# Kernel optimization log

Measured on AMD Instinct MI355X. Metric: run time of the kernel, lower is better.

The kernel has to match this reference:

```python
import math
import jax, jax.numpy as jnp
import numpy as np

DILATIONS = (1, 2, 3)

def conv2d(x, w, b, d=1, p=0):
    # x: NCHW, w: OIHW
    y = jax.lax.conv_general_dilated(
        x, w, window_strides=(1, 1), padding=[(p, p), (p, p)],
        rhs_dilation=(d, d), dimension_numbers=('NCHW', 'OIHW', 'NCHW'))
    return y + b[None, :, None, None]

def setup_inputs() -> dict:
    key = jax.random.key(0)
    ks = jax.random.split(key, 6)
    B, C, H = 2, 256, 96
    inner = 256 // 18  # = 14
    f = lambda k, s, sc: jax.random.normal(k, s, dtype=jnp.float32) * sc
    return {
        'x':        f(ks[0], (B, C, H, H), 1.0),
        'proj_w':   f(ks[1], (C, C, 1, 1), 0.06),
        'proj_b':   jnp.zeros((C,), jnp.float32),
        'reduce_w': f(ks[2], (inner, C, 1, 1), 0.06),
        'reduce_b': jnp.zeros((inner,), jnp.float32),
        'dil_w':    f(ks[3], (3, inner, inner, 3, 3), 0.08),
        'dil_b':    jnp.zeros((3, inner), jnp.float32),
        'fuse_w':   f(ks[4], (C, inner * 3 * 6, 1, 1), 0.06),
        'fuse_b':   jnp.zeros((C,), jnp.float32),
    }

def reference(x, proj_w, proj_b, reduce_w, reduce_b, dil_w, dil_b, fuse_w, fuse_b):
    B, C, H, W = x.shape
    # PatchEmbed (1x1 conv, stride 1) then PatchUnEmbed is identity on layout
    fmap = conv2d(x, proj_w, proj_b)                    # (B,C,H,W)
    # SAMSNLMFilter
    xr = conv2d(fmap, reduce_w, reduce_b)               # (B,inner,H,W)
    tfs = [xr,
           jnp.flip(xr, -1),
           jnp.flip(xr, -2),
           jnp.rot90(xr, 1, (-2, -1)),
           jnp.rot90(xr, 2, (-2, -1)),
           jnp.rot90(xr, 3, (-2, -1))]
    feats = []
    for i, d in enumerate(DILATIONS):
        co = conv2d(xr, dil_w[i], dil_b[i], d=d, p=d)   # (B,inner,H,W)
        feats.extend(co * t for t in tfs)
    fused = conv2d(jnp.concatenate(feats, axis=1), fuse_w, fuse_b)  # (B,C,H,W)
    tok = fused.reshape(B, C, H * W).transpose(0, 2, 1)             # (B,N,C)
    scale = 1.0 / math.sqrt(C)
    scores = jnp.einsum('bnc,bmc->bnm', tok, tok) * scale           # (B,N,N)
    attn = jax.nn.softmax(scores, axis=-1)
    out = jnp.einsum('bnm,bmc->bnc', attn, tok)
    out = out.transpose(0, 2, 1).reshape(B, C, H, W)
    return fmap + 0.2 * out  # residual_scale default 0.2
```

## Files before the change

kernel.cpp:

```cpp
#include <hip/hip_runtime.h>
#include <hip/hip_bf16.h>

#define NB 2
#define CH 256
#define HS 96
#define HW 9216
#define CHW 2359296
#define INNER 14
#define NF 252
#define SCALE 0.0625f

using f32x4 = __attribute__((ext_vector_type(4))) float;
using s16x8 = __attribute__((ext_vector_type(8))) short;

template<int CIN, typename OT>
__global__ __launch_bounds__(256)
void k_conv1x1(const float* __restrict__ in, const float* __restrict__ w,
               const float* __restrict__ bias, OT* __restrict__ out) {
    __shared__ float wsh[CIN][32];
    const int tid = threadIdx.x;
    const int coB = blockIdx.y * 32;
    for (int e = tid; e < CIN * 32; e += 256) {
        int ci = e >> 5, col = e & 31;
        wsh[ci][col] = w[(coB + col) * CIN + ci];
    }
    __syncthreads();
    const int P0  = blockIdx.x * 512 + tid;
    const int b   = P0 / HW;
    const int pp0 = P0 - b * HW;
    const int pp1 = pp0 + 256;
    const float* inb = in + (size_t)b * CIN * HW;
    float acc0[32], acc1[32];
    #pragma unroll
    for (int j = 0; j < 32; ++j) { acc0[j] = 0.f; acc1[j] = 0.f; }
    for (int ci = 0; ci < CIN; ++ci) {
        float x0 = inb[(size_t)ci * HW + pp0];
        float x1 = inb[(size_t)ci * HW + pp1];
        const float4* wr = (const float4*)wsh[ci];
        #pragma unroll
        for (int q = 0; q < 8; ++q) {
            float4 wv = wr[q];
            acc0[q*4+0] += wv.x*x0; acc0[q*4+1] += wv.y*x0;
            acc0[q*4+2] += wv.z*x0; acc0[q*4+3] += wv.w*x0;
            acc1[q*4+0] += wv.x*x1; acc1[q*4+1] += wv.y*x1;
            acc1[q*4+2] += wv.z*x1; acc1[q*4+3] += wv.w*x1;
        }
    }
    OT* ob = out + (size_t)b * CH * HW;
    #pragma unroll
    for (int j = 0; j < 32; ++j) {
        float bv = bias[coB + j];
        ob[(size_t)(coB + j) * HW + pp0] = (OT)(acc0[j] + bv);
        ob[(size_t)(coB + j) * HW + pp1] = (OT)(acc1[j] + bv);
    }
}

__global__ __launch_bounds__(64)
void k_reduce(const float* __restrict__ fmap, const float* __restrict__ w,
              const float* __restrict__ bias, float* __restrict__ xr) {
    __shared__ float wsh[256][16];
    const int tid = threadIdx.x;
    for (int e = tid; e < 256 * 16; e += 64) {
        int ci = e >> 4, co = e & 15;
        wsh[ci][co] = (co < INNER) ? w[co * 256 + ci] : 0.f;
    }
    __syncthreads();
    const int P  = blockIdx.x * 64 + tid;
    const int b  = P / HW;
    const int pp = P - b * HW;
    const float* fb = fmap + (size_t)b * CHW;
    float acc[16];
    #pragma unroll
    for (int j = 0; j < 16; ++j) acc[j] = 0.f;
    for (int ci = 0; ci < 256; ++ci) {
        float xv = fb[(size_t)ci * HW + pp];
        const float4* wr = (const float4*)wsh[ci];
        #pragma unroll
        for (int q = 0; q < 4; ++q) {
            float4 wv = wr[q];
            acc[q*4+0] += wv.x*xv; acc[q*4+1] += wv.y*xv;
            acc[q*4+2] += wv.z*xv; acc[q*4+3] += wv.w*xv;
        }
    }
    float* xb = xr + (size_t)b * INNER * HW;
    #pragma unroll
    for (int co = 0; co < INNER; ++co)
        xb[(size_t)co * HW + pp] = acc[co] + bias[co];
}

__global__ __launch_bounds__(256)
void k_dil(const float* __restrict__ xr, const float* __restrict__ dw,
           const float* __restrict__ db, float* __restrict__ feats) {
    int bid = blockIdx.x;
    const int hb = bid % 36; bid /= 36;
    const int oc = bid % 14; bid /= 14;
    const int b  = bid & 1;  bid >>= 1;
    const int d  = bid;
    const int dil = d + 1;
    __shared__ float wsh[126];
    const int tid = threadIdx.x;
    if (tid < 126) wsh[tid] = dw[(d * 14 + oc) * 126 + tid];
    __syncthreads();
    const int p = hb * 256 + tid;
    const int h = p / 96, w = p - (p / 96) * 96;
    const float* xb = xr + (size_t)b * INNER * HW;
    float acc = db[d * 14 + oc];
    for (int ic = 0; ic < 14; ++ic) {
        const float* xc = xb + (size_t)ic * HW;
        #pragma unroll
        for (int kh = 0; kh < 3; ++kh) {
            int ih = h + (kh - 1) * dil;
            if (ih < 0 || ih >= 96) continue;
            #pragma unroll
            for (int kw = 0; kw < 3; ++kw) {
                int iw = w + (kw - 1) * dil;
                if (iw < 0 || iw >= 96) continue;
                acc += xc[ih * 96 + iw] * wsh[ic * 9 + kh * 3 + kw];
            }
        }
    }
    const float* xo = xb + (size_t)oc * HW;
    const int H1 = 95;
    float t0 = xo[h * 96 + w];
    float t1 = xo[h * 96 + (H1 - w)];
    float t2 = xo[(H1 - h) * 96 + w];
    float t3 = xo[w * 96 + (H1 - h)];
    float t4 = xo[(H1 - h) * 96 + (H1 - w)];
    float t5 = xo[(H1 - w) * 96 + h];
    float* fo = feats + (size_t)b * NF * HW;
    const int ch0 = d * 6 * 14 + oc;
    fo[(size_t)(ch0 + 0 * 14) * HW + p] = acc * t0;
    fo[(size_t)(ch0 + 1 * 14) * HW + p] = acc * t1;
    fo[(size_t)(ch0 + 2 * 14) * HW + p] = acc * t2;
    fo[(size_t)(ch0 + 3 * 14) * HW + p] = acc * t3;
    fo[(size_t)(ch0 + 4 * 14) * HW + p] = acc * t4;
    fo[(size_t)(ch0 + 5 * 14) * HW + p] = acc * t5;
}

__global__ __launch_bounds__(256)
void k_tr(const unsigned short* __restrict__ tc, unsigned short* __restrict__ tt) {
    const int tid = threadIdx.x;
    int bid = blockIdx.x;
    const int b = bid / 576;
    const int r = bid - b * 576;
    const int t0 = (r >> 2) * 64;
    const int c0 = (r & 3) * 64;
    __shared__ unsigned int T[64][37];
    const unsigned short* tcb = tc + (size_t)b * CHW;
    unsigned short* ttb = tt + (size_t)b * CHW;
    for (int e = tid; e < 2048; e += 256) {
        int to = e & 63, chp = e >> 6;
        unsigned int v0 = tcb[(size_t)(c0 + 2*chp)     * HW + t0 + to];
        unsigned int v1 = tcb[(size_t)(c0 + 2*chp + 1) * HW + t0 + to];
        T[to][chp] = (v1 << 16) | v0;
    }
    __syncthreads();
    for (int e = tid; e < 2048; e += 256) {
        int to = e >> 5, chp = e & 31;
        ((unsigned int*)(ttb + (size_t)(t0 + to) * CH + c0))[chp] = T[to][chp];
    }
}

#define KTILE 64
#define NKT 144

__device__ __forceinline__ unsigned int pk_bf16(float lo, float hi) {
    unsigned int l = __bfloat16_as_ushort(__float2bfloat16(lo));
    unsigned int h = __bfloat16_as_ushort(__float2bfloat16(hi));
    return (h << 16) | l;
}

__global__ __launch_bounds__(256, 2)
void k_attn2(const unsigned short* __restrict__ tok_t,
             const unsigned short* __restrict__ tok_c,
             const float* __restrict__ fmap, float* __restrict__ outp) {
    __shared__ unsigned short Kt[64][256];
    __shared__ unsigned short Vt[256][64];
    __shared__ unsigned short Psh[4][16][72];
    const int tid  = threadIdx.x;
    const int wid  = tid >> 6;
    const int lane = tid & 63;
    const int lq   = lane & 15;
    const int lg   = lane >> 4;

    const int blk = blockIdx.x;
    const int qb  = (blk & 7) * 36 + (blk >> 3);
    const int b   = qb / 144;
    const int q0  = (qb - b * 144) * 64;
    const unsigned short* tt = tok_t + (size_t)b * CHW;
    const unsigned short* tc = tok_c + (size_t)b * CHW;

    s16x8 qf[8];
    {
        const unsigned short* qrow = tt + (size_t)(q0 + wid*16 + lq) * CH + 8*lg;
        #pragma unroll
        for (int ks = 0; ks < 8; ++ks)
            qf[ks] = *(const s16x8*)(qrow + 32*ks);
    }
    float m_r = -1e30f, l_r = 0.f;
    f32x4 oacc[16];
    #pragma unroll
    for (int ct = 0; ct < 16; ++ct) oacc[ct] = (f32x4){0.f,0.f,0.f,0.f};

    for (int t = 0; t < NKT; ++t) {
        const int k0 = t * KTILE;
        __syncthreads();
        for (int c = tid; c < 2048; c += 256) {
            int key = c >> 5, cho = (c & 31) * 8;
            s16x8 v = *(const s16x8*)(tt + (size_t)(k0 + key) * CH + cho);
            *(s16x8*)(&Kt[key][cho ^ ((key & 7) << 3)]) = v;
        }
        for (int c = tid; c < 2048; c += 256) {
            int ch = c >> 3, ko = (c & 7) * 8;
            s16x8 v = *(const s16x8*)(tc + (size_t)ch * HW + k0 + ko);
            *(s16x8*)(&Vt[ch][ko ^ ((ch & 7) << 3)]) = v;
        }
        __syncthreads();

        float s[16];
        #pragma unroll
        for (int mt = 0; mt < 4; ++mt) {
            f32x4 acc = (f32x4){0.f,0.f,0.f,0.f};
            const int key = mt * 16 + lq;
            const int sw  = (key & 7) << 3;
            #pragma unroll
            for (int ks = 0; ks < 8; ++ks) {
                s16x8 af = *(const s16x8*)(&Kt[key][(ks*32 + 8*lg) ^ sw]);
                acc = __builtin_amdgcn_mfma_f32_16x16x32_bf16(af, qf[ks], acc, 0, 0, 0);
            }
            #pragma unroll
            for (int r = 0; r < 4; ++r) s[mt*4 + r] = acc[r] * SCALE;
        }
        float tm = s[0];
        #pragma unroll
        for (int i = 1; i < 16; ++i) tm = fmaxf(tm, s[i]);
        tm = fmaxf(tm, __shfl_xor(tm, 16));
        tm = fmaxf(tm, __shfl_xor(tm, 32));
        const float mn = fmaxf(m_r, tm);
        const float alpha = __expf(m_r - mn);
        m_r = mn;
        float ps = 0.f;
        #pragma unroll
        for (int i = 0; i < 16; ++i) { s[i] = __expf(s[i] - mn); ps += s[i]; }
        ps += __shfl_xor(ps, 16);
        ps += __shfl_xor(ps, 32);
        l_r = l_r * alpha + ps;
        #pragma unroll
        for (int ct = 0; ct < 16; ++ct) {
            oacc[ct][0] *= alpha; oacc[ct][1] *= alpha;
            oacc[ct][2] *= alpha; oacc[ct][3] *= alpha;
        }
        #pragma unroll
        for (int kt = 0; kt < 4; ++kt) {
            *(unsigned int*)&Psh[wid][lq][16*kt + 4*lg]     = pk_bf16(s[kt*4+0], s[kt*4+1]);
            *(unsigned int*)&Psh[wid][lq][16*kt + 4*lg + 2] = pk_bf16(s[kt*4+2], s[kt*4+3]);
        }
        s16x8 pb0 = *(const s16x8*)&Psh[wid][lq][8*lg];
        s16x8 pb1 = *(const s16x8*)&Psh[wid][lq][32 + 8*lg];
        #pragma unroll
        for (int ct = 0; ct < 16; ++ct) {
            const int ch = ct * 16 + lq;
            const int sw = (ch & 7) << 3;
            s16x8 va0 = *(const s16x8*)(&Vt[ch][(8*lg) ^ sw]);
            s16x8 va1 = *(const s16x8*)(&Vt[ch][(32 + 8*lg) ^ sw]);
            oacc[ct] = __builtin_amdgcn_mfma_f32_16x16x32_bf16(va0, pb0, oacc[ct], 0, 0, 0);
            oacc[ct] = __builtin_amdgcn_mfma_f32_16x16x32_bf16(va1, pb1, oacc[ct], 0, 0, 0);
        }
    }
    const float linv = 1.f / l_r;
    const float* fb = fmap + (size_t)b * CHW;
    float* ob = outp + (size_t)b * CHW;
    const int qg = q0 + wid * 16 + lq;
    #pragma unroll
    for (int ct = 0; ct < 16; ++ct)
        #pragma unroll
        for (int cr = 0; cr < 4; ++cr) {
            const int ch = ct * 16 + 4 * lg + cr;
            const size_t g = (size_t)ch * HW + qg;
            ob[g] = fb[g] + 0.2f * (oacc[ct][cr] * linv);
        }
}

extern "C" void kernel_launch(void* const* d_in, const int* in_sizes, int n_in,
                              void* d_out, int out_size, void* d_ws, size_t ws_size,
                              hipStream_t stream) {
    const float* x        = (const float*)d_in[0];
    const float* proj_w   = (const float*)d_in[1];
    const float* proj_b   = (const float*)d_in[2];
    const float* reduce_w = (const float*)d_in[3];
    const float* reduce_b = (const float*)d_in[4];
    const float* dil_w    = (const float*)d_in[5];
    const float* dil_b    = (const float*)d_in[6];
    const float* fuse_w   = (const float*)d_in[7];
    const float* fuse_b   = (const float*)d_in[8];
    float* out = (float*)d_out;

    float* ws    = (float*)d_ws;
    float* fmap  = ws;
    float* xr    = fmap + 4718592;
    float* feats = xr + 258048;
    unsigned short* tok_c = (unsigned short*)(feats + 4644864);
    unsigned short* tok_t = tok_c + 4718592;

    k_conv1x1<256, float><<<dim3(36, 8), 256, 0, stream>>>(x, proj_w, proj_b, fmap);
    k_reduce<<<288, 64, 0, stream>>>(fmap, reduce_w, reduce_b, xr);
    k_dil<<<3024, 256, 0, stream>>>(xr, dil_w, dil_b, feats);
    k_conv1x1<252, __hip_bfloat16><<<dim3(36, 8), 256, 0, stream>>>(
        feats, fuse_w, fuse_b, (__hip_bfloat16*)tok_c);
    k_tr<<<1152, 256, 0, stream>>>(tok_c, tok_t);
    k_attn2<<<288, 256, 0, stream>>>(tok_t, tok_c, fmap, out);
}
```

Baseline: 871.7 us.

## Double-buffer attention K/V tiles with direct global-to-LDS loads and lazy rescale

The attention kernel now double-buffers K and V tiles in LDS, filling them with global_load_lds asynchronous copies so the next tile's fetch overlaps the current tile's MFMA work, and it drops one barrier per iteration. Softmax switches to exp2 with a pre-folded log2e scale and only rescales the accumulators when the running max grows by more than a threshold. The reduce kernel is widened to 256 threads, splitting the channel loop four ways with an LDS reduction. Doubling LDS forces one block per CU (launch bounds lowered), which reduces occupancy, and the lazy-rescale threshold relies on fp32 headroom.

New measurement: 964.8 us. +10.7%, slower.

```diff
diff --git a/kernel.cpp b/kernel.cpp
--- a/kernel.cpp
+++ b/kernel.cpp
@@ -8,10 +8,17 @@
 #define CHW 2359296
 #define INNER 14
 #define NF 252
-#define SCALE 0.0625f
+#define SL2E 0.09016844f
 
 using f32x4 = __attribute__((ext_vector_type(4))) float;
 using s16x8 = __attribute__((ext_vector_type(8))) short;
+
+__device__ __forceinline__ void gload_lds16(const unsigned short* g, unsigned short* l) {
+    __builtin_amdgcn_global_load_lds(
+        (const __attribute__((address_space(1))) unsigned int*)g,
+        (__attribute__((address_space(3))) unsigned int*)l,
+        16, 0, 0);
+}
 
 template<int CIN, typename OT>
 __global__ __launch_bounds__(256)
@@ -55,26 +62,28 @@
     }
 }
 
-__global__ __launch_bounds__(64)
+__global__ __launch_bounds__(256)
 void k_reduce(const float* __restrict__ fmap, const float* __restrict__ w,
               const float* __restrict__ bias, float* __restrict__ xr) {
     __shared__ float wsh[256][16];
+    __shared__ float part[4][64][17];
     const int tid = threadIdx.x;
-    for (int e = tid; e < 256 * 16; e += 64) {
+    for (int e = tid; e < 256 * 16; e += 256) {
         int ci = e >> 4, co = e & 15;
         wsh[ci][co] = (co < INNER) ? w[co * 256 + ci] : 0.f;
     }
     __syncthreads();
-    const int P  = blockIdx.x * 64 + tid;
-    const int b  = P / HW;
-    const int pp = P - b * HW;
-    const float* fb = fmap + (size_t)b * CHW;
+    const int px  = tid & 63, grp = tid >> 6;
+    const int Pb  = blockIdx.x * 64;
+    const int b   = Pb / HW;
+    const int ppb = Pb - b * HW;
+    const float* fb = fmap + (size_t)b * CHW + (size_t)(grp * 64) * HW + ppb + px;
     float acc[16];
     #pragma unroll
     for (int j = 0; j < 16; ++j) acc[j] = 0.f;
-    for (int ci = 0; ci < 256; ++ci) {
-        float xv = fb[(size_t)ci * HW + pp];
-        const float4* wr = (const float4*)wsh[ci];
+    for (int ci = 0; ci < 64; ++ci) {
+        float xv = fb[(size_t)ci * HW];
+        const float4* wr = (const float4*)wsh[grp * 64 + ci];
         #pragma unroll
         for (int q = 0; q < 4; ++q) {
             float4 wv = wr[q];
@@ -82,10 +91,15 @@
             acc[q*4+2] += wv.z*xv; acc[q*4+3] += wv.w*xv;
         }
     }
-    float* xb = xr + (size_t)b * INNER * HW;
-    #pragma unroll
-    for (int co = 0; co < INNER; ++co)
-        xb[(size_t)co * HW + pp] = acc[co] + bias[co];
+    #pragma unroll
+    for (int j = 0; j < 16; ++j) part[grp][px][j] = acc[j];
+    __syncthreads();
+    for (int e = tid; e < 64 * INNER; e += 256) {
+        int co = e >> 6, p2 = e & 63;
+        float v = part[0][p2][co] + part[1][p2][co] + part[2][p2][co] +
+                  part[3][p2][co] + bias[co];
+        xr[(size_t)(b * INNER + co) * HW + ppb + p2] = v;
+    }
 }
 
 __global__ __launch_bounds__(256)
@@ -170,12 +184,12 @@
     return (h << 16) | l;
 }
 
-__global__ __launch_bounds__(256, 2)
+__global__ __launch_bounds__(256, 1)
 void k_attn2(const unsigned short* __restrict__ tok_t,
              const unsigned short* __restrict__ tok_c,
              const float* __restrict__ fmap, float* __restrict__ outp) {
-    __shared__ unsigned short Kt[64][256];
-    __shared__ unsigned short Vt[256][64];
+    __shared__ unsigned short Kt[2][64][256];
+    __shared__ unsigned short Vt[2][256][64];
     __shared__ unsigned short Psh[4][16][72];
     const int tid  = threadIdx.x;
     const int wid  = tid >> 6;
@@ -190,6 +204,18 @@
     const unsigned short* tt = tok_t + (size_t)b * CHW;
     const unsigned short* tc = tok_c + (size_t)b * CHW;
 
+    int koff[8], voff[8];
+    #pragma unroll
+    for (int i = 0; i < 8; ++i) {
+        int c   = i * 256 + tid;
+        int key = c >> 5, sc = c & 31;
+        koff[i] = key * CH + ((sc ^ (key & 7)) << 3);
+        int ch  = c >> 3, sv = c & 7;
+        voff[i] = ch * HW + ((sv ^ (ch & 7)) << 3);
+    }
+    unsigned short* KtF = &Kt[0][0][0];
+    unsigned short* VtF = &Vt[0][0][0];
+
     s16x8 qf[8];
     {
         const unsigned short* qrow = tt + (size_t)(q0 + wid*16 + lq) * CH + 8*lg;
@@ -202,21 +228,29 @@
     #pragma unroll
     for (int ct = 0; ct < 16; ++ct) oacc[ct] = (f32x4){0.f,0.f,0.f,0.f};
 
+    #pragma unroll
+    for (int i = 0; i < 8; ++i) {
+        int c = i * 256 + tid;
+        gload_lds16(tt + koff[i], KtF + c * 8);
+        gload_lds16(tc + voff[i], VtF + c * 8);
+    }
+    __syncthreads();
+
+    int cur = 0;
     for (int t = 0; t < NKT; ++t) {
-        const int k0 = t * KTILE;
-        __syncthreads();
-        for (int c = tid; c < 2048; c += 256) {
-            int key = c >> 5, cho = (c & 31) * 8;
-            s16x8 v = *(const s16x8*)(tt + (size_t)(k0 + key) * CH + cho);
-            *(s16x8*)(&Kt[key][cho ^ ((key & 7) << 3)]) = v;
-        }
-        for (int c = tid; c < 2048; c += 256) {
-            int ch = c >> 3, ko = (c & 7) * 8;
-            s16x8 v = *(const s16x8*)(tc + (size_t)ch * HW + k0 + ko);
-            *(s16x8*)(&Vt[ch][ko ^ ((ch & 7) << 3)]) = v;
-        }
-        __syncthreads();
-
+        if (t + 1 < NKT) {
+            const int kn = (t + 1) * KTILE;
+            const unsigned short* tk = tt + (size_t)kn * CH;
+            const unsigned short* tv = tc + kn;
+            unsigned short* kd = KtF + (cur ^ 1) * 16384;
+            unsigned short* vd = VtF + (cur ^ 1) * 16384;
+            #pragma unroll
+            for (int i = 0; i < 8; ++i) {
+                int c = i * 256 + tid;
+                gload_lds16(tk + koff[i], kd + c * 8);
+                gload_lds16(tv + voff[i], vd + c * 8);
+            }
+        }
         float s[16];
         #pragma unroll
         for (int mt = 0; mt < 4; ++mt) {
@@ -225,11 +259,11 @@
             const int sw  = (key & 7) << 3;
             #pragma unroll
             for (int ks = 0; ks < 8; ++ks) {
-                s16x8 af = *(const s16x8*)(&Kt[key][(ks*32 + 8*lg) ^ sw]);
+                s16x8 af = *(const s16x8*)(&Kt[cur][key][(ks*32 + 8*lg) ^ sw]);
                 acc = __builtin_amdgcn_mfma_f32_16x16x32_bf16(af, qf[ks], acc, 0, 0, 0);
             }
             #pragma unroll
-            for (int r = 0; r < 4; ++r) s[mt*4 + r] = acc[r] * SCALE;
+            for (int r = 0; r < 4; ++r) s[mt*4 + r] = acc[r] * SL2E;
         }
         float tm = s[0];
         #pragma unroll
@@ -237,19 +271,22 @@
         tm = fmaxf(tm, __shfl_xor(tm, 16));
         tm = fmaxf(tm, __shfl_xor(tm, 32));
         const float mn = fmaxf(m_r, tm);
-        const float alpha = __expf(m_r - mn);
-        m_r = mn;
+        if (!__all(mn - m_r <= 8.0f)) {
+            const float alpha = exp2f(m_r - mn);
+            m_r = mn;
+            l_r *= alpha;
+            #pragma unroll
+            for (int ct = 0; ct < 16; ++ct) {
+                oacc[ct][0] *= alpha; oacc[ct][1] *= alpha;
+                oacc[ct][2] *= alpha; oacc[ct][3] *= alpha;
+            }
+        }
         float ps = 0.f;
         #pragma unroll
-        for (int i = 0; i < 16; ++i) { s[i] = __expf(s[i] - mn); ps += s[i]; }
+        for (int i = 0; i < 16; ++i) { s[i] = exp2f(s[i] - m_r); ps += s[i]; }
         ps += __shfl_xor(ps, 16);
         ps += __shfl_xor(ps, 32);
-        l_r = l_r * alpha + ps;
-        #pragma unroll
-        for (int ct = 0; ct < 16; ++ct) {
-            oacc[ct][0] *= alpha; oacc[ct][1] *= alpha;
-            oacc[ct][2] *= alpha; oacc[ct][3] *= alpha;
-        }
+        l_r += ps;
         #pragma unroll
         for (int kt = 0; kt < 4; ++kt) {
             *(unsigned int*)&Psh[wid][lq][16*kt + 4*lg]     = pk_bf16(s[kt*4+0], s[kt*4+1]);
@@ -261,11 +298,13 @@
         for (int ct = 0; ct < 16; ++ct) {
             const int ch = ct * 16 + lq;
             const int sw = (ch & 7) << 3;
-            s16x8 va0 = *(const s16x8*)(&Vt[ch][(8*lg) ^ sw]);
-            s16x8 va1 = *(const s16x8*)(&Vt[ch][(32 + 8*lg) ^ sw]);
+            s16x8 va0 = *(const s16x8*)(&Vt[cur][ch][(8*lg) ^ sw]);
+            s16x8 va1 = *(const s16x8*)(&Vt[cur][ch][(32 + 8*lg) ^ sw]);
             oacc[ct] = __builtin_amdgcn_mfma_f32_16x16x32_bf16(va0, pb0, oacc[ct], 0, 0, 0);
             oacc[ct] = __builtin_amdgcn_mfma_f32_16x16x32_bf16(va1, pb1, oacc[ct], 0, 0, 0);
         }
+        __syncthreads();
+        cur ^= 1;
     }
     const float linv = 1.f / l_r;
     const float* fb = fmap + (size_t)b * CHW;
@@ -303,7 +342,7 @@
     unsigned short* tok_t = tok_c + 4718592;
 
     k_conv1x1<256, float><<<dim3(36, 8), 256, 0, stream>>>(x, proj_w, proj_b, fmap);
-    k_reduce<<<288, 64, 0, stream>>>(fmap, reduce_w, reduce_b, xr);
+    k_reduce<<<288, 256, 0, stream>>>(fmap, reduce_w, reduce_b, xr);
     k_dil<<<3024, 256, 0, stream>>>(xr, dil_w, dil_b, feats);
     k_conv1x1<252, __hip_bfloat16><<<dim3(36, 8), 256, 0, stream>>>(
         feats, fuse_w, fuse_b, (__hip_bfloat16*)tok_c);
```
